# Performance work log

Measured on AMD Instinct MI355X. Metric: run time of the kernel, lower is better.

The kernel has to match this reference:

```python
import jax, jax.numpy as jnp
import numpy as np
import math

M, DIN, DTGT = 65536, 256, 256   # feature count and feature dims
S, SD_IN, SD_TGT = 64, 256, 256  # num_slots, in_slot_dim, tgt_slot_dim
ITERS = 3
H_IN = 128                        # mlp_in hidden (hardcoded 128 in source)
H_TGT = SD_TGT if SD_TGT > 128 else 128  # mlp_tgt hidden

ARGS = ["inputs", "target", "in_slots", "tgt_slots",
        "ln_in_g", "ln_in_b", "ln_tgt_g", "ln_tgt_b",
        "Wk", "bk", "Wv", "bv", "Wvt", "bvt",
        "ln_slots_g", "ln_slots_b", "Wq", "bq",
        "gru_in_Wih", "gru_in_Whh", "gru_in_bih", "gru_in_bhh",
        "gru_tgt_Wih", "gru_tgt_Whh", "gru_tgt_bih", "gru_tgt_bhh",
        "ln_mi_g", "ln_mi_b", "mi_W1", "mi_b1", "mi_W2", "mi_b2",
        "ln_mt_g", "ln_mt_b", "mt_W1", "mt_b1", "mt_W2", "mt_b2"]


def _ln(x, g, b):
    m = jnp.mean(x, axis=-1, keepdims=True)
    v = jnp.var(x, axis=-1, keepdims=True)
    return (x - m) * jax.lax.rsqrt(v + 1e-5) * g + b


def _gru(x, h, Wih, Whh, bih, bhh):
    # torch.nn.GRUCell semantics; Wih: (D, 3H), Whh: (H, 3H)
    H = h.shape[-1]
    gi = x @ Wih + bih
    gh = h @ Whh + bhh
    r = jax.nn.sigmoid(gi[:, :H] + gh[:, :H])
    z = jax.nn.sigmoid(gi[:, H:2 * H] + gh[:, H:2 * H])
    n = jnp.tanh(gi[:, 2 * H:] + r * gh[:, 2 * H:])
    return (1.0 - z) * n + z * h


def _forward(inputs, target, in_slots, tgt_slots,
             ln_in_g, ln_in_b, ln_tgt_g, ln_tgt_b,
             Wk, bk, Wv, bv, Wvt, bvt,
             ln_slots_g, ln_slots_b, Wq, bq,
             gru_in_Wih, gru_in_Whh, gru_in_bih, gru_in_bhh,
             gru_tgt_Wih, gru_tgt_Whh, gru_tgt_bih, gru_tgt_bhh,
             ln_mi_g, ln_mi_b, mi_W1, mi_b1, mi_W2, mi_b2,
             ln_mt_g, ln_mt_b, mt_W1, mt_b1, mt_W2, mt_b2):
    inputs_norm = _ln(inputs, ln_in_g, ln_in_b)          # [M, DIN]
    in_k = inputs_norm @ Wk + bk                          # [M, SD_IN]
    in_v = inputs_norm @ Wv + bv                          # [M, SD_IN]
    tgt_v = _ln(target, ln_tgt_g, ln_tgt_b) @ Wvt + bvt   # [M, SD_TGT]
    scale = 1.0 / math.sqrt(in_k.shape[1])
    attn = None
    for _ in range(ITERS):
        q = _ln(in_slots, ln_slots_g, ln_slots_b) @ Wq + bq   # [S, SD_IN]
        logits = (q @ in_k.T) * scale                          # [S, M]
        attn = jax.nn.softmax(logits, axis=0)                  # softmax over SLOTS (dim=0)
        in_up = attn @ in_v                                    # [S, SD_IN]
        tgt_up = attn @ tgt_v                                  # [S, SD_TGT]
        in_slots = _gru(in_up, in_slots, gru_in_Wih, gru_in_Whh, gru_in_bih, gru_in_bhh)
        tgt_slots = _gru(tgt_up, tgt_slots, gru_tgt_Wih, gru_tgt_Whh, gru_tgt_bih, gru_tgt_bhh)
        in_slots = in_slots + (jax.nn.relu(_ln(in_slots, ln_mi_g, ln_mi_b) @ mi_W1 + mi_b1) @ mi_W2 + mi_b2)
        tgt_slots = tgt_slots + (jax.nn.relu(_ln(tgt_slots, ln_mt_g, ln_mt_b) @ mt_W1 + mt_b1) @ mt_W2 + mt_b2)
    return (in_slots, tgt_slots, attn)


def setup_inputs() -> dict:
    key = jax.random.key(0)
    ks = iter(jax.random.split(key, 64))
    rn = lambda shape, s=1.0: jax.random.normal(next(ks), shape, dtype=jnp.float32) * s
    w = 0.02
    d = {
        "inputs": rn((M, DIN)),
        "target": rn((M, DTGT)),
        "in_slots": rn((S, SD_IN)),
        "tgt_slots": rn((S, SD_TGT)),
        "ln_in_g": jnp.ones((DIN,)), "ln_in_b": jnp.zeros((DIN,)),
        "ln_tgt_g": jnp.ones((DTGT,)), "ln_tgt_b": jnp.zeros((DTGT,)),
        "Wk": rn((DIN, SD_IN), w), "bk": jnp.zeros((SD_IN,)),
        "Wv": rn((DIN, SD_IN), w), "bv": jnp.zeros((SD_IN,)),
        "Wvt": rn((DTGT, SD_TGT), w), "bvt": jnp.zeros((SD_TGT,)),
        "ln_slots_g": jnp.ones((SD_IN,)), "ln_slots_b": jnp.zeros((SD_IN,)),
        "Wq": rn((SD_IN, SD_IN), w), "bq": jnp.zeros((SD_IN,)),
        "gru_in_Wih": rn((SD_IN, 3 * SD_IN), w), "gru_in_Whh": rn((SD_IN, 3 * SD_IN), w),
        "gru_in_bih": jnp.zeros((3 * SD_IN,)), "gru_in_bhh": jnp.zeros((3 * SD_IN,)),
        "gru_tgt_Wih": rn((SD_TGT, 3 * SD_TGT), w), "gru_tgt_Whh": rn((SD_TGT, 3 * SD_TGT), w),
        "gru_tgt_bih": jnp.zeros((3 * SD_TGT,)), "gru_tgt_bhh": jnp.zeros((3 * SD_TGT,)),
        "ln_mi_g": jnp.ones((SD_IN,)), "ln_mi_b": jnp.zeros((SD_IN,)),
        "mi_W1": rn((SD_IN, H_IN), w), "mi_b1": jnp.zeros((H_IN,)),
        "mi_W2": rn((H_IN, SD_IN), w), "mi_b2": jnp.zeros((SD_IN,)),
        "ln_mt_g": jnp.ones((SD_TGT,)), "ln_mt_b": jnp.zeros((SD_TGT,)),
        "mt_W1": rn((SD_TGT, H_TGT), w), "mt_b1": jnp.zeros((H_TGT,)),
        "mt_W2": rn((H_TGT, SD_TGT), w), "mt_b2": jnp.zeros((SD_TGT,)),
    }
    return {k: d[k] for k in ARGS}


def reference(inputs, target, in_slots, tgt_slots,
              ln_in_g, ln_in_b, ln_tgt_g, ln_tgt_b,
              Wk, bk, Wv, bv, Wvt, bvt,
              ln_slots_g, ln_slots_b, Wq, bq,
              gru_in_Wih, gru_in_Whh, gru_in_bih, gru_in_bhh,
              gru_tgt_Wih, gru_tgt_Whh, gru_tgt_bih, gru_tgt_bhh,
              ln_mi_g, ln_mi_b, mi_W1, mi_b1, mi_W2, mi_b2,
              ln_mt_g, ln_mt_b, mt_W1, mt_b1, mt_W2, mt_b2):
    return _forward(inputs, target, in_slots, tgt_slots,
                    ln_in_g, ln_in_b, ln_tgt_g, ln_tgt_b,
                    Wk, bk, Wv, bv, Wvt, bvt,
                    ln_slots_g, ln_slots_b, Wq, bq,
                    gru_in_Wih, gru_in_Whh, gru_in_bih, gru_in_bhh,
                    gru_tgt_Wih, gru_tgt_Whh, gru_tgt_bih, gru_tgt_bhh,
                    ln_mi_g, ln_mi_b, mi_W1, mi_b1, mi_W2, mi_b2,
                    ln_mt_g, ln_mt_b, mt_W1, mt_b1, mt_W2, mt_b2)
```

## Files before the change

kernel.cpp:

```cpp
#include <hip/hip_runtime.h>
#include <hip/hip_bf16.h>
#include <math.h>

typedef __bf16 bf16_t;
typedef __bf16 bf16x8 __attribute__((ext_vector_type(8)));
typedef __bf16 bf16x4 __attribute__((ext_vector_type(4)));
typedef float f32x4 __attribute__((ext_vector_type(4)));

#define DEVI __device__ __forceinline__

DEVI f32x4 mfma16(bf16x8 a, bf16x8 b, f32x4 c) {
  return __builtin_amdgcn_mfma_f32_16x16x32_bf16(a, b, c, 0, 0, 0);
}
DEVI bf16x8 ld8(const bf16_t* p) { return *reinterpret_cast<const bf16x8*>(p); }


struct WtArgs { const float* s0; const float* s1; const float* s2; const float* s3;
                const float* s4; const float* s5; const float* s6; const float* s7;
                const float* s8; const float* s9; const float* s10; const float* s11; };

__global__ __launch_bounds__(256) void k_wtrans(WtArgs A, bf16_t* __restrict__ wt,
                                                const float* __restrict__ g_in,
                                                const float* __restrict__ g_tgt) {
  constexpr int offs[12] = {0,65536,131072,196608,262144,458752,655360,851968,
                            1048576,1081344,1114112,1179648};
  constexpr int Ks[12]   = {256,256,256,256,256,256,256,256,256,128,256,256};
  constexpr int Ns[12]   = {256,256,256,256,768,768,768,768,128,256,256,256};
  const int m = blockIdx.y;
  const int K = Ks[m], N = Ns[m];
  const int tn = N >> 6;
  const int tile = blockIdx.x;
  if (tile >= (K >> 6) * tn) return;
  const int tk = tile / tn, tc = tile - tk * tn;
  const float* sp;
  switch (m) {
    case 0: sp = A.s0; break; case 1: sp = A.s1; break; case 2: sp = A.s2; break;
    case 3: sp = A.s3; break; case 4: sp = A.s4; break; case 5: sp = A.s5; break;
    case 6: sp = A.s6; break; case 7: sp = A.s7; break; case 8: sp = A.s8; break;
    case 9: sp = A.s9; break; case 10: sp = A.s10; break; default: sp = A.s11; break;
  }
  const float* gv = (m == 2) ? g_tgt : ((m < 2) ? g_in : nullptr);
  __shared__ float ts[64][65];
  const int t = threadIdx.x;
  const int k0 = tk * 64, n0 = tc * 64;
  {
    const int c = t & 63, rq = t >> 6;
    #pragma unroll
    for (int i = 0; i < 16; ++i) {
      const int r = rq * 16 + i;
      float val = sp[(size_t)(k0 + r) * N + n0 + c];
      if (gv) val *= gv[k0 + r];
      ts[r][c] = val;
    }
  }
  __syncthreads();
  bf16_t* dst = wt + offs[m];
  const int n_l = t & 63, kq = t >> 6;
  #pragma unroll
  for (int h = 0; h < 2; ++h) {
    const int k_l = kq * 16 + h * 8;
    bf16x8 pk;
    #pragma unroll
    for (int e = 0; e < 8; ++e) pk[e] = (bf16_t)ts[k_l + e][n_l];
    const int n_g = n0 + n_l, k_g = k0 + k_l;
    const int nt = n_g >> 4, kc = k_g >> 5;
    const int lane = (((k_g >> 3) & 3) << 4) + (n_g & 15);
    *reinterpret_cast<bf16x8*>(dst + (((size_t)(nt * (K >> 5) + kc)) << 9) + lane * 8) = pk;
  }
}

__global__ __launch_bounds__(256) void k_bias(
    const float* __restrict__ Wk, const float* __restrict__ Wv, const float* __restrict__ Wvt,
    const float* __restrict__ b_in, const float* __restrict__ b_tgt,
    const float* __restrict__ bk, const float* __restrict__ bv, const float* __restrict__ bvt,
    float* __restrict__ out) {
  const int which = blockIdx.x;
  const float* W = which == 0 ? Wk : (which == 1 ? Wv : Wvt);
  const float* bvec = which == 2 ? b_tgt : b_in;
  const float* bias = which == 0 ? bk : (which == 1 ? bv : bvt);
  const int n = threadIdx.x;
  float sum = bias[n];
  for (int k = 0; k < 256; ++k) sum += bvec[k] * W[(size_t)k * 256 + n];
  out[which * 256 + n] = sum;
}

__global__ __launch_bounds__(256) void k_init(const float* __restrict__ in_slots,
                                              const float* __restrict__ tgt_slots,
                                              float* __restrict__ h_f32,
                                              bf16_t* __restrict__ h_bf) {
  int idx = blockIdx.x * 256 + threadIdx.x;
  int side = idx >> 14, j = idx & 16383;
  int s = j >> 8, d = j & 255;
  float x = (side ? tgt_slots : in_slots)[j];
  h_f32[idx] = x;
  h_bf[side*16384 + (((s>>4)*8 + (d>>5))<<9) + ((d>>3)&3)*128 + (s&15)*8 + (d&7)] = (bf16_t)x;
}

DEVI void gemm_pass(const bf16_t* aFl, const bf16_t* __restrict__ WF,
                    int w, int l, f32x4 acc[4][4]) {
  #pragma unroll 1
  for (int ks = 0; ks < 8; ++ks) {
    bf16x8 a[4], b[4];
    #pragma unroll
    for (int mt = 0; mt < 4; ++mt) a[mt] = ld8(aFl + ((mt*8 + ks) << 9) + l*8);
    #pragma unroll
    for (int dt = 0; dt < 4; ++dt) b[dt] = ld8(WF + (((size_t)((w*4 + dt)*8 + ks)) << 9) + l*8);
    #pragma unroll
    for (int mt = 0; mt < 4; ++mt)
      #pragma unroll
      for (int dt = 0; dt < 4; ++dt) acc[mt][dt] = mfma16(a[mt], b[dt], acc[mt][dt]);
  }
}

__global__ __launch_bounds__(256) void k_phaseA(
    const float* __restrict__ inputs, const float* __restrict__ target,
    const bf16_t* __restrict__ wkF, const bf16_t* __restrict__ wvF, const bf16_t* __restrict__ wvtF,
    const float* __restrict__ bfold,
    bf16_t* __restrict__ in_kF, bf16_t* __restrict__ in_vF, bf16_t* __restrict__ tgt_vF) {
  const int side = blockIdx.y;
  const int m0 = blockIdx.x * 64;
  const int t = threadIdx.x, l = t & 63, w = t >> 6;
  const int l16 = l & 15, l4 = l >> 4;
  __shared__ __align__(16) bf16_t aF[16384];

  {
    const float* src = side ? target : inputs;
    const int row = m0 + w*16 + l16;
    const float* srcp = src + (size_t)row * 256 + l4 * 8;
    float4 xa[8], xb[8];
    #pragma unroll
    for (int j = 0; j < 8; ++j) {
      xa[j] = *reinterpret_cast<const float4*>(srcp + j*32);
      xb[j] = *reinterpret_cast<const float4*>(srcp + j*32 + 4);
    }
    float s1 = 0.f, s2 = 0.f;
    #pragma unroll
    for (int j = 0; j < 8; ++j) {
      s1 += xa[j].x + xa[j].y + xa[j].z + xa[j].w + xb[j].x + xb[j].y + xb[j].z + xb[j].w;
      s2 += xa[j].x*xa[j].x + xa[j].y*xa[j].y + xa[j].z*xa[j].z + xa[j].w*xa[j].w
          + xb[j].x*xb[j].x + xb[j].y*xb[j].y + xb[j].z*xb[j].z + xb[j].w*xb[j].w;
    }
    s1 += __shfl_xor(s1, 16); s1 += __shfl_xor(s1, 32);
    s2 += __shfl_xor(s2, 16); s2 += __shfl_xor(s2, 32);
    const float mean = s1 * (1.f/256.f);
    const float rstd = rsqrtf(s2 * (1.f/256.f) - mean*mean + 1e-5f);
    #pragma unroll
    for (int j = 0; j < 8; ++j) {
      bf16x8 pk;
      pk[0] = (bf16_t)((xa[j].x - mean) * rstd);
      pk[1] = (bf16_t)((xa[j].y - mean) * rstd);
      pk[2] = (bf16_t)((xa[j].z - mean) * rstd);
      pk[3] = (bf16_t)((xa[j].w - mean) * rstd);
      pk[4] = (bf16_t)((xb[j].x - mean) * rstd);
      pk[5] = (bf16_t)((xb[j].y - mean) * rstd);
      pk[6] = (bf16_t)((xb[j].z - mean) * rstd);
      pk[7] = (bf16_t)((xb[j].w - mean) * rstd);
      *reinterpret_cast<bf16x8*>(aF + ((w*8 + j) << 9) + l*8) = pk;
    }
  }
  __syncthreads();

  if (side == 0) {
    {
      f32x4 acc[4][4] = {};
      gemm_pass(aF, wkF, w, l, acc);
      #pragma unroll
      for (int mt = 0; mt < 4; ++mt) {
        const int mtg = blockIdx.x*4 + mt;
        #pragma unroll
        for (int dt = 0; dt < 4; ++dt) {
          const int dtg = w*4 + dt;
          const float bias = bfold[dtg*16 + l16];
          bf16_t* bp = in_kF + (((size_t)(mtg*8 + (dtg>>1))) << 9)
                       + ((dtg&1)*2 + (l16>>3))*128 + (l16&7);
          #pragma unroll
          for (int rr = 0; rr < 4; ++rr)
            bp[(l4*4 + rr)*8] = (bf16_t)(acc[mt][dt][rr] + bias);
        }
      }
    }
    {
      f32x4 acc[4][4] = {};
      gemm_pass(aF, wvF, w, l, acc);
      #pragma unroll
      for (int mt = 0; mt < 4; ++mt) {
        const int mcg = blockIdx.x*2 + (mt>>1);
        #pragma unroll
        for (int dt = 0; dt < 4; ++dt) {
          const int dtg = w*4 + dt;
          const float bias = bfold[256 + dtg*16 + l16];
          bf16x4 pk;
          #pragma unroll
          for (int rr = 0; rr < 4; ++rr) pk[rr] = (bf16_t)(acc[mt][dt][rr] + bias);
          *reinterpret_cast<bf16x4*>(in_vF + (((size_t)(dtg*2048 + mcg)) << 9)
              + ((mt&1)*2 + (l4>>1))*128 + l16*8 + (l4&1)*4) = pk;
        }
      }
    }
  } else {
    f32x4 acc[4][4] = {};
    gemm_pass(aF, wvtF, w, l, acc);
    #pragma unroll
    for (int mt = 0; mt < 4; ++mt) {
      const int mcg = blockIdx.x*2 + (mt>>1);
      #pragma unroll
      for (int dt = 0; dt < 4; ++dt) {
        const int dtg = w*4 + dt;
        const float bias = bfold[512 + dtg*16 + l16];
        bf16x4 pk;
        #pragma unroll
        for (int rr = 0; rr < 4; ++rr) pk[rr] = (bf16_t)(acc[mt][dt][rr] + bias);
        *reinterpret_cast<bf16x4*>(tgt_vF + (((size_t)(dtg*2048 + mcg)) << 9)
            + ((mt&1)*2 + (l4>>1))*128 + l16*8 + (l4&1)*4) = pk;
      }
    }
  }
}

__global__ __launch_bounds__(256) void k_q(
    const float* __restrict__ h_in,
    const float* __restrict__ ln_g, const float* __restrict__ ln_b,
    const bf16_t* __restrict__ wqF, const float* __restrict__ bq,
    bf16_t* __restrict__ q_bf) {
  __shared__ __align__(16) bf16_t anorm[64][264];
  const int t = threadIdx.x, l = t & 63, w = t >> 6;
  const float4 g4 = *reinterpret_cast<const float4*>(ln_g + l * 4);
  const float4 b4 = *reinterpret_cast<const float4*>(ln_b + l * 4);
  float4 v[16];
  #pragma unroll
  for (int i = 0; i < 16; ++i)
    v[i] = *reinterpret_cast<const float4*>(h_in + (size_t)(w*16 + i) * 256 + l * 4);
  #pragma unroll
  for (int i = 0; i < 16; ++i) {
    float s1 = v[i].x + v[i].y + v[i].z + v[i].w;
    float s2 = v[i].x*v[i].x + v[i].y*v[i].y + v[i].z*v[i].z + v[i].w*v[i].w;
    #pragma unroll
    for (int msk = 1; msk < 64; msk <<= 1) { s1 += __shfl_xor(s1, msk); s2 += __shfl_xor(s2, msk); }
    const float mean = s1 * (1.f/256.f);
    const float rstd = rsqrtf(s2 * (1.f/256.f) - mean*mean + 1e-5f);
    bf16x4 pk;
    pk[0] = (bf16_t)((v[i].x - mean) * rstd * g4.x + b4.x);
    pk[1] = (bf16_t)((v[i].y - mean) * rstd * g4.y + b4.y);
    pk[2] = (bf16_t)((v[i].z - mean) * rstd * g4.z + b4.z);
    pk[3] = (bf16_t)((v[i].w - mean) * rstd * g4.w + b4.w);
    *reinterpret_cast<bf16x4*>(&anorm[w*16 + i][l*4]) = pk;
  }
  __syncthreads();
  const int l16 = l & 15, l4 = l >> 4;
  f32x4 acc[4][4] = {};
  for (int ks = 0; ks < 8; ++ks) {
    const int k = ks*32 + l4*8;
    bf16x8 a[4], b[4];
    #pragma unroll
    for (int mi = 0; mi < 4; ++mi) a[mi] = ld8(&anorm[mi*16 + l16][k]);
    #pragma unroll
    for (int ni = 0; ni < 4; ++ni) b[ni] = ld8(wqF + (((size_t)((w*4 + ni)*8 + ks)) << 9) + l*8);
    #pragma unroll
    for (int mi = 0; mi < 4; ++mi)
      #pragma unroll
      for (int ni = 0; ni < 4; ++ni) acc[mi][ni] = mfma16(a[mi], b[ni], acc[mi][ni]);
  }
  #pragma unroll
  for (int mi = 0; mi < 4; ++mi)
    #pragma unroll
    for (int ni = 0; ni < 4; ++ni) {
      const int d = w*64 + ni*16 + l16;
      const float bias = bq[d];
      bf16_t* outp = q_bf + (((size_t)(mi*8 + w*2 + (ni>>1))) << 9) + ((ni&1)*2 + (l16>>3))*128 + (l16&7);
      #pragma unroll
      for (int rr = 0; rr < 4; ++rr)
        outp[(l4*4 + rr)*8] = (bf16_t)((acc[mi][ni][rr] + bias) * 0.0625f);
    }
}

__global__ __launch_bounds__(256) void k_logits(
    const bf16_t* __restrict__ q_bf, const bf16_t* __restrict__ in_kF,
    bf16_t* __restrict__ attnF, float* __restrict__ attn_f32, int write_f32) {
  __shared__ __align__(16) bf16_t stg[4][64][68];
  const int t = threadIdx.x, l = t & 63, w = t >> 6, l16 = l & 15, l4 = l >> 4;
  const int m0 = blockIdx.x * 256 + w * 64;
  f32x4 acc[4][4] = {};
  for (int ks = 0; ks < 8; ++ks) {
    bf16x8 a[4], b[4];
    #pragma unroll
    for (int mi = 0; mi < 4; ++mi) a[mi] = ld8(q_bf + (((size_t)(mi*8 + ks)) << 9) + l*8);
    #pragma unroll
    for (int ni = 0; ni < 4; ++ni)
      b[ni] = ld8(in_kF + (((size_t)((blockIdx.x*16 + w*4 + ni)*8 + ks)) << 9) + l*8);
    #pragma unroll
    for (int mi = 0; mi < 4; ++mi)
      #pragma unroll
      for (int ni = 0; ni < 4; ++ni) acc[mi][ni] = mfma16(a[mi], b[ni], acc[mi][ni]);
  }
  #pragma unroll
  for (int ni = 0; ni < 4; ++ni) {
    float mx = -3.0e38f;
    #pragma unroll
    for (int mi = 0; mi < 4; ++mi)
      #pragma unroll
      for (int rr = 0; rr < 4; ++rr) mx = fmaxf(mx, acc[mi][ni][rr]);
    mx = fmaxf(mx, __shfl_xor(mx, 16));
    mx = fmaxf(mx, __shfl_xor(mx, 32));
    float sm = 0.f;
    #pragma unroll
    for (int mi = 0; mi < 4; ++mi)
      #pragma unroll
      for (int rr = 0; rr < 4; ++rr) {
        float ev = __expf(acc[mi][ni][rr] - mx);
        acc[mi][ni][rr] = ev; sm += ev;
      }
    sm += __shfl_xor(sm, 16);
    sm += __shfl_xor(sm, 32);
    const float inv = 1.0f / sm;
    #pragma unroll
    for (int mi = 0; mi < 4; ++mi)
      #pragma unroll
      for (int rr = 0; rr < 4; ++rr) acc[mi][ni][rr] *= inv;
  }
  #pragma unroll
  for (int mi = 0; mi < 4; ++mi)
    #pragma unroll
    for (int ni = 0; ni < 4; ++ni)
      #pragma unroll
      for (int rr = 0; rr < 4; ++rr) {
        stg[w][mi*16 + l4*4 + rr][ni*16 + l16] = (bf16_t)acc[mi][ni][rr];
        if (write_f32) {
          const int s = mi*16 + l4*4 + rr;
          attn_f32[(size_t)s*65536 + (m0 + ni*16 + l16)] = acc[mi][ni][rr];
        }
      }
  #pragma unroll
  for (int mi = 0; mi < 4; ++mi)
    #pragma unroll
    for (int mc = 0; mc < 2; ++mc) {
      bf16x8 vv = *reinterpret_cast<const bf16x8*>(&stg[w][mi*16 + l16][mc*32 + l4*8]);
      *reinterpret_cast<bf16x8*>(attnF +
          ((((size_t)mi)*2048 + (blockIdx.x*8 + w*2 + mc)) << 9) + l*8) = vv;
    }
}

__global__ __launch_bounds__(256) void k_pv(
    const bf16_t* __restrict__ attnF,
    const bf16_t* __restrict__ in_vF, const bf16_t* __restrict__ tgt_vF,
    bf16_t* __restrict__ p_in, bf16_t* __restrict__ p_tgt) {
  const int c = blockIdx.x, side = blockIdx.y;
  const bf16_t* V = side ? tgt_vF : in_vF;
  bf16_t* P = side ? p_tgt : p_in;
  const int t = threadIdx.x, l = t & 63, w = t >> 6, l16 = l & 15, l4 = l >> 4;
  f32x4 acc[4][4] = {};
  for (int ks = 0; ks < 16; ++ks) {
    const size_t mc = c*16 + ks;
    bf16x8 a[4], b[4];
    #pragma unroll
    for (int mi = 0; mi < 4; ++mi) a[mi] = ld8(attnF + ((((size_t)mi)*2048 + mc) << 9) + l*8);
    #pragma unroll
    for (int ni = 0; ni < 4; ++ni) b[ni] = ld8(V + ((((size_t)(w*4 + ni))*2048 + mc) << 9) + l*8);
    #pragma unroll
    for (int mi = 0; mi < 4; ++mi)
      #pragma unroll
      for (int ni = 0; ni < 4; ++ni) acc[mi][ni] = mfma16(a[mi], b[ni], acc[mi][ni]);
  }
  #pragma unroll
  for (int mi = 0; mi < 4; ++mi)
    #pragma unroll
    for (int ni = 0; ni < 4; ++ni) {
      const int d = w*64 + ni*16 + l16;
      #pragma unroll
      for (int rr = 0; rr < 4; ++rr) {
        const int s = mi*16 + l4*4 + rr;
        P[(size_t)c*16384 + s*256 + d] = (bf16_t)acc[mi][ni][rr];
      }
    }
}

__global__ __launch_bounds__(256) void k_pvred(
    const bf16_t* __restrict__ p_in, const bf16_t* __restrict__ p_tgt,
    bf16_t* __restrict__ upF) {
  const int b = blockIdx.x;
  const int side = b >> 6, s = b & 63;
  const int d = threadIdx.x;
  const bf16_t* P = (side ? p_tgt : p_in) + s*256 + d;
  float sum = 0.f;
  #pragma unroll 8
  for (int cc = 0; cc < 128; ++cc) sum += (float)P[(size_t)cc * 16384];
  upF[side*16384 + (((s>>4)*8 + (d>>5))<<9) + ((d>>3)&3)*128 + (s&15)*8 + (d&7)] = (bf16_t)sum;
}

__global__ __launch_bounds__(256) void k_gates(
    const bf16_t* __restrict__ upF, const bf16_t* __restrict__ h_bf,
    const bf16_t* __restrict__ wihF_in, const bf16_t* __restrict__ whhF_in,
    const bf16_t* __restrict__ wihF_tgt, const bf16_t* __restrict__ whhF_tgt,
    const float* __restrict__ bih_in, const float* __restrict__ bhh_in,
    const float* __restrict__ bih_tgt, const float* __restrict__ bhh_tgt,
    float* __restrict__ gi, float* __restrict__ gh) {
  const int nchunk = blockIdx.x, which = blockIdx.y, side = blockIdx.z;
  const bf16_t* Aop = (which ? h_bf : upF) + side*16384;
  const bf16_t* WF = side ? (which ? whhF_tgt : wihF_tgt) : (which ? whhF_in : wihF_in);
  const float* bias = side ? (which ? bhh_tgt : bih_tgt) : (which ? bhh_in : bih_in);
  float* out = (which ? gh : gi) + side*49152;
  const int t = threadIdx.x, l = t & 63, w = t >> 6, l16 = l & 15, l4 = l >> 4;
  const int n0 = nchunk*256 + w*64;
  f32x4 acc[4][4] = {};
  for (int ks = 0; ks < 8; ++ks) {
    bf16x8 a[4], b[4];
    #pragma unroll
    for (int mi = 0; mi < 4; ++mi) a[mi] = ld8(Aop + (((size_t)(mi*8 + ks)) << 9) + l*8);
    #pragma unroll
    for (int ni = 0; ni < 4; ++ni)
      b[ni] = ld8(WF + (((size_t)((nchunk*16 + w*4 + ni)*8 + ks)) << 9) + l*8);
    #pragma unroll
    for (int mi = 0; mi < 4; ++mi)
      #pragma unroll
      for (int ni = 0; ni < 4; ++ni) acc[mi][ni] = mfma16(a[mi], b[ni], acc[mi][ni]);
  }
  #pragma unroll
  for (int mi = 0; mi < 4; ++mi)
    #pragma unroll
    for (int ni = 0; ni < 4; ++ni) {
      const int n = n0 + ni*16 + l16;
      const float bb = bias[n];
      #pragma unroll
      for (int rr = 0; rr < 4; ++rr) {
        const int s = mi*16 + l4*4 + rr;
        out[(size_t)s*768 + n] = acc[mi][ni][rr] + bb;
      }
    }
}

__global__ __launch_bounds__(256) void k_gru_ln(
    const float* __restrict__ gi, const float* __restrict__ gh,
    const float* __restrict__ h_f32,
    const float* __restrict__ ln_mi_g, const float* __restrict__ ln_mi_b,
    const float* __restrict__ ln_mt_g, const float* __restrict__ ln_mt_b,
    float* __restrict__ hp_f32, bf16_t* __restrict__ hpnF) {
  const int s = blockIdx.x, side = blockIdx.y;
  const int d = threadIdx.x;
  const float* GI = gi + side*49152 + s*768;
  const float* GH = gh + side*49152 + s*768;
  const float hv = h_f32[side*16384 + s*256 + d];
  const float rg = 1.f / (1.f + __expf(-(GI[d] + GH[d])));
  const float zg = 1.f / (1.f + __expf(-(GI[256 + d] + GH[256 + d])));
  const float ng = tanhf(GI[512 + d] + rg * GH[512 + d]);
  const float hp = (1.f - zg) * ng + zg * hv;
  float a = hp, b2 = hp * hp;
  #pragma unroll
  for (int msk = 1; msk < 64; msk <<= 1) { a += __shfl_xor(a, msk); b2 += __shfl_xor(b2, msk); }
  __shared__ float reda[4], redb[4];
  const int w = d >> 6, lid = d & 63;
  if (lid == 0) { reda[w] = a; redb[w] = b2; }
  __syncthreads();
  const float S1 = reda[0] + reda[1] + reda[2] + reda[3];
  const float S2 = redb[0] + redb[1] + redb[2] + redb[3];
  const float mean = S1 * (1.f/256.f);
  const float rstd = rsqrtf(S2 * (1.f/256.f) - mean*mean + 1e-5f);
  const float* g = side ? ln_mt_g : ln_mi_g;
  const float* bb = side ? ln_mt_b : ln_mi_b;
  const float nv = (hp - mean) * rstd * g[d] + bb[d];
  hp_f32[side*16384 + s*256 + d] = hp;
  hpnF[side*16384 + (((s>>4)*8 + (d>>5))<<9) + ((d>>3)&3)*128 + (s&15)*8 + (d&7)] = (bf16_t)nv;
}

__global__ __launch_bounds__(256) void k_mlpq(
    const bf16_t* __restrict__ hpnF,
    const bf16_t* __restrict__ w1F_in, const bf16_t* __restrict__ w1F_tgt,
    const float* __restrict__ b1_in, const float* __restrict__ b1_tgt,
    const bf16_t* __restrict__ w2F_in, const bf16_t* __restrict__ w2F_tgt,
    const float* __restrict__ b2_in, const float* __restrict__ b2_tgt,
    const float* __restrict__ hp_f32,
    float* __restrict__ h_f32, bf16_t* __restrict__ h_bf, float* __restrict__ slots_out,
    const float* __restrict__ ln_sg, const float* __restrict__ ln_sb,
    const bf16_t* __restrict__ wqF, const float* __restrict__ bq,
    bf16_t* __restrict__ q_bf, int make_q) {
  const int side = blockIdx.x;
  __shared__ __align__(16) bf16_t hid[64][264];
  const int t = threadIdx.x, l = t & 63, w = t >> 6, l16 = l & 15, l4 = l >> 4;
  const int NH = side ? 256 : 128;
  {
    const bf16_t* Aop = hpnF + side*16384;
    const bf16_t* WF = side ? w1F_tgt : w1F_in;
    const float* b1 = side ? b1_tgt : b1_in;
    const int ntiles = NH >> 6;
    for (int nt = 0; nt < ntiles; ++nt) {
      const int n0 = w*(NH>>2) + nt*16;
      f32x4 acc[4] = {};
      for (int ks = 0; ks < 8; ++ks) {
        bf16x8 b = ld8(WF + (((size_t)((n0>>4)*8 + ks)) << 9) + l*8);
        #pragma unroll
        for (int mt = 0; mt < 4; ++mt)
          acc[mt] = mfma16(ld8(Aop + (((size_t)(mt*8 + ks)) << 9) + l*8), b, acc[mt]);
      }
      const float bb = b1[n0 + l16];
      #pragma unroll
      for (int mt = 0; mt < 4; ++mt)
        #pragma unroll
        for (int rr = 0; rr < 4; ++rr) {
          const int s = mt*16 + l4*4 + rr;
          hid[s][n0 + l16] = (bf16_t)fmaxf(acc[mt][rr] + bb, 0.f);
        }
    }
  }
  __syncthreads();
  {
    const bf16_t* WF = side ? w2F_tgt : w2F_in;
    const float* b2 = side ? b2_tgt : b2_in;
    const int ksteps = NH >> 5;
    #pragma unroll
    for (int nt = 0; nt < 4; ++nt) {
      const int n0 = w*64 + nt*16;
      f32x4 acc[4] = {};
      for (int ks = 0; ks < ksteps; ++ks) {
        const int k = ks*32 + l4*8;
        bf16x8 b = ld8(WF + (((size_t)((n0>>4)*ksteps + ks)) << 9) + l*8);
        #pragma unroll
        for (int mt = 0; mt < 4; ++mt)
          acc[mt] = mfma16(ld8(&hid[mt*16 + l16][k]), b, acc[mt]);
      }
      const int n = n0 + l16;
      const float bb = b2[n];
      #pragma unroll
      for (int mt = 0; mt < 4; ++mt)
        #pragma unroll
        for (int rr = 0; rr < 4; ++rr) {
          const int s = mt*16 + l4*4 + rr;
          const int idx = side*16384 + s*256 + n;
          const float val = acc[mt][rr] + bb + hp_f32[idx];
          h_f32[idx] = val;
          slots_out[idx] = val;
          h_bf[side*16384 + (((s>>4)*8 + (n>>5))<<9) + ((n>>3)&3)*128 + (s&15)*8 + (n&7)] = (bf16_t)val;
        }
    }
  }
  if (!make_q || side != 0) return;
  __syncthreads();
  {
    for (int i = 0; i < 16; ++i) {
      const int s = w*16 + i;
      float4 x = *reinterpret_cast<const float4*>(h_f32 + s*256 + 4*l);
      float a = x.x + x.y + x.z + x.w;
      float b2s = x.x*x.x + x.y*x.y + x.z*x.z + x.w*x.w;
      #pragma unroll
      for (int msk = 1; msk < 64; msk <<= 1) { a += __shfl_xor(a, msk); b2s += __shfl_xor(b2s, msk); }
      const float mean = a * (1.f/256.f);
      const float rstd = rsqrtf(b2s * (1.f/256.f) - mean*mean + 1e-5f);
      float4 g4 = *reinterpret_cast<const float4*>(ln_sg + 4*l);
      float4 bb4 = *reinterpret_cast<const float4*>(ln_sb + 4*l);
      bf16x4 pk;
      pk[0] = (bf16_t)((x.x - mean) * rstd * g4.x + bb4.x);
      pk[1] = (bf16_t)((x.y - mean) * rstd * g4.y + bb4.y);
      pk[2] = (bf16_t)((x.z - mean) * rstd * g4.z + bb4.z);
      pk[3] = (bf16_t)((x.w - mean) * rstd * g4.w + bb4.w);
      *reinterpret_cast<bf16x4*>(&hid[s][4*l]) = pk;
    }
  }
  __syncthreads();
  {
    #pragma unroll
    for (int nt = 0; nt < 4; ++nt) {
      const int n0 = w*64 + nt*16;
      f32x4 acc[4] = {};
      for (int ks = 0; ks < 8; ++ks) {
        const int k = ks*32 + l4*8;
        bf16x8 b = ld8(wqF + (((size_t)((n0>>4)*8 + ks)) << 9) + l*8);
        #pragma unroll
        for (int mt = 0; mt < 4; ++mt)
          acc[mt] = mfma16(ld8(&hid[mt*16 + l16][k]), b, acc[mt]);
      }
      const int d = n0 + l16;
      const float bb = bq[d];
      #pragma unroll
      for (int mt = 0; mt < 4; ++mt) {
        bf16_t* op = q_bf + (((size_t)(mt*8 + (d>>5))) << 9) + ((d>>3)&3)*128 + (d&7);
        #pragma unroll
        for (int rr = 0; rr < 4; ++rr)
          op[(l4*4 + rr)*8] = (bf16_t)((acc[mt][rr] + bb) * 0.0625f);
      }
    }
  }
}

extern "C" void kernel_launch(void* const* d_in, const int* in_sizes, int n_in,
                              void* d_out, int out_size, void* d_ws, size_t ws_size,
                              hipStream_t stream) {
  (void)in_sizes; (void)n_in; (void)out_size; (void)ws_size;
  const float* inputs     = (const float*)d_in[0];
  const float* target     = (const float*)d_in[1];
  const float* in_slots   = (const float*)d_in[2];
  const float* tgt_slots  = (const float*)d_in[3];
  const float* ln_in_g    = (const float*)d_in[4];
  const float* ln_in_b    = (const float*)d_in[5];
  const float* ln_tgt_g   = (const float*)d_in[6];
  const float* ln_tgt_b   = (const float*)d_in[7];
  const float* Wk  = (const float*)d_in[8];
  const float* bk  = (const float*)d_in[9];
  const float* Wv  = (const float*)d_in[10];
  const float* bv  = (const float*)d_in[11];
  const float* Wvt = (const float*)d_in[12];
  const float* bvt = (const float*)d_in[13];
  const float* ln_slots_g = (const float*)d_in[14];
  const float* ln_slots_b = (const float*)d_in[15];
  const float* Wq  = (const float*)d_in[16];
  const float* bq  = (const float*)d_in[17];
  const float* gru_in_Wih  = (const float*)d_in[18];
  const float* gru_in_Whh  = (const float*)d_in[19];
  const float* gru_in_bih  = (const float*)d_in[20];
  const float* gru_in_bhh  = (const float*)d_in[21];
  const float* gru_tgt_Wih = (const float*)d_in[22];
  const float* gru_tgt_Whh = (const float*)d_in[23];
  const float* gru_tgt_bih = (const float*)d_in[24];
  const float* gru_tgt_bhh = (const float*)d_in[25];
  const float* ln_mi_g = (const float*)d_in[26];
  const float* ln_mi_b = (const float*)d_in[27];
  const float* mi_W1 = (const float*)d_in[28];
  const float* mi_b1 = (const float*)d_in[29];
  const float* mi_W2 = (const float*)d_in[30];
  const float* mi_b2 = (const float*)d_in[31];
  const float* ln_mt_g = (const float*)d_in[32];
  const float* ln_mt_b = (const float*)d_in[33];
  const float* mt_W1 = (const float*)d_in[34];
  const float* mt_b1 = (const float*)d_in[35];
  const float* mt_W2 = (const float*)d_in[36];
  const float* mt_b2 = (const float*)d_in[37];

  char* ws = (char*)d_ws;
  bf16_t* wt      = (bf16_t*)(ws);
  bf16_t* in_kF   = (bf16_t*)(ws + 2490368ull);
  bf16_t* in_vF   = (bf16_t*)(ws + 36044800ull);
  bf16_t* tgt_vF  = (bf16_t*)(ws + 69599232ull);
  bf16_t* attnF   = (bf16_t*)(ws + 103153664ull);
  bf16_t* q_bf    = (bf16_t*)(ws + 111542272ull);
  bf16_t* h_bf    = (bf16_t*)(ws + 111575040ull);
  bf16_t* upF     = (bf16_t*)(ws + 111640576ull);
  bf16_t* hpnF    = (bf16_t*)(ws + 111673344ull);
  float*  h_f32   = (float*)(ws + 111706112ull);
  float*  hp_f32  = (float*)(ws + 111837184ull);
  float*  gi      = (float*)(ws + 111968256ull);
  float*  gh      = (float*)(ws + 112361472ull);
  bf16_t* p_in    = (bf16_t*)(ws + 112754688ull);
  bf16_t* p_tgt   = (bf16_t*)(ws + 116948992ull);
  float*  bfold   = (float*)(ws + 121143296ull);

  bf16_t* wkF = wt;
  bf16_t* wvF = wt + 65536;
  bf16_t* wvtF = wt + 131072;
  bf16_t* wqF = wt + 196608;
  bf16_t* wihF_in  = wt + 262144;
  bf16_t* whhF_in  = wt + 458752;
  bf16_t* wihF_tgt = wt + 655360;
  bf16_t* whhF_tgt = wt + 851968;
  bf16_t* w1F_in  = wt + 1048576;
  bf16_t* w2F_in  = wt + 1081344;
  bf16_t* w1F_tgt = wt + 1114112;
  bf16_t* w2F_tgt = wt + 1179648;

  float* attn_out = (float*)d_out + 32768;

  WtArgs wa = {Wk, Wv, Wvt, Wq, gru_in_Wih, gru_in_Whh, gru_tgt_Wih, gru_tgt_Whh,
               mi_W1, mi_W2, mt_W1, mt_W2};
  k_wtrans<<<dim3(48, 12), 256, 0, stream>>>(wa, wt, ln_in_g, ln_tgt_g);
  k_bias<<<3, 256, 0, stream>>>(Wk, Wv, Wvt, ln_in_b, ln_tgt_b, bk, bv, bvt, bfold);
  k_init<<<128, 256, 0, stream>>>(in_slots, tgt_slots, h_f32, h_bf);
  k_phaseA<<<dim3(1024, 2), 256, 0, stream>>>(inputs, target,
      wkF, wvF, wvtF, bfold, in_kF, in_vF, tgt_vF);
  k_q<<<1, 256, 0, stream>>>(h_f32, ln_slots_g, ln_slots_b, wqF, bq, q_bf);

  for (int it = 0; it < 3; ++it) {
    k_logits<<<256, 256, 0, stream>>>(q_bf, in_kF, attnF, attn_out, it == 2 ? 1 : 0);
    k_pv<<<dim3(128, 2), 256, 0, stream>>>(attnF, in_vF, tgt_vF, p_in, p_tgt);
    k_pvred<<<128, 256, 0, stream>>>(p_in, p_tgt, upF);
    k_gates<<<dim3(3, 2, 2), 256, 0, stream>>>(upF, h_bf, wihF_in, whhF_in,
        wihF_tgt, whhF_tgt, gru_in_bih, gru_in_bhh, gru_tgt_bih, gru_tgt_bhh, gi, gh);
    k_gru_ln<<<dim3(64, 2), 256, 0, stream>>>(gi, gh, h_f32, ln_mi_g, ln_mi_b,
        ln_mt_g, ln_mt_b, hp_f32, hpnF);
    k_mlpq<<<2, 256, 0, stream>>>(hpnF, w1F_in, w1F_tgt, mi_b1, mt_b1,
        w2F_in, w2F_tgt, mi_b2, mt_b2, hp_f32, h_f32, h_bf, (float*)d_out,
        ln_slots_g, ln_slots_b, wqF, bq, q_bf, it < 2 ? 1 : 0);
  }
}
```

Before: 322.6 us.

## Fuse logits/softmax with PV matmul and enlarge phaseA row tile

```diff
diff --git a/kernel.cpp b/kernel.cpp
--- a/kernel.cpp
+++ b/kernel.cpp
@@ -96,19 +96,19 @@
   h_bf[side*16384 + (((s>>4)*8 + (d>>5))<<9) + ((d>>3)&3)*128 + (s&15)*8 + (d&7)] = (bf16_t)x;
 }
 
-DEVI void gemm_pass(const bf16_t* aFl, const bf16_t* __restrict__ WF,
-                    int w, int l, f32x4 acc[4][4]) {
+DEVI void gemm_pass8(const bf16_t* aFl, const bf16_t* __restrict__ WF,
+                     int w, int l, f32x4 acc[8][4]) {
   #pragma unroll 1
   for (int ks = 0; ks < 8; ++ks) {
-    bf16x8 a[4], b[4];
-    #pragma unroll
-    for (int mt = 0; mt < 4; ++mt) a[mt] = ld8(aFl + ((mt*8 + ks) << 9) + l*8);
+    bf16x8 b[4];
     #pragma unroll
     for (int dt = 0; dt < 4; ++dt) b[dt] = ld8(WF + (((size_t)((w*4 + dt)*8 + ks)) << 9) + l*8);
     #pragma unroll
-    for (int mt = 0; mt < 4; ++mt)
-      #pragma unroll
-      for (int dt = 0; dt < 4; ++dt) acc[mt][dt] = mfma16(a[mt], b[dt], acc[mt][dt]);
+    for (int mt = 0; mt < 8; ++mt) {
+      bf16x8 a = ld8(aFl + ((mt*8 + ks) << 9) + l*8);
+      #pragma unroll
+      for (int dt = 0; dt < 4; ++dt) acc[mt][dt] = mfma16(a, b[dt], acc[mt][dt]);
+    }
   }
 }
 
@@ -118,14 +118,15 @@
     const float* __restrict__ bfold,
     bf16_t* __restrict__ in_kF, bf16_t* __restrict__ in_vF, bf16_t* __restrict__ tgt_vF) {
   const int side = blockIdx.y;
-  const int m0 = blockIdx.x * 64;
+  const int m0 = blockIdx.x * 128;
   const int t = threadIdx.x, l = t & 63, w = t >> 6;
   const int l16 = l & 15, l4 = l >> 4;
-  __shared__ __align__(16) bf16_t aF[16384];
-
-  {
-    const float* src = side ? target : inputs;
-    const int row = m0 + w*16 + l16;
+  __shared__ __align__(16) bf16_t aF[32768];
+
+  const float* src = side ? target : inputs;
+  #pragma unroll 1
+  for (int p = 0; p < 2; ++p) {
+    const int row = m0 + p*64 + w*16 + l16;
     const float* srcp = src + (size_t)row * 256 + l4 * 8;
     float4 xa[8], xb[8];
     #pragma unroll
@@ -155,18 +156,18 @@
       pk[5] = (bf16_t)((xb[j].y - mean) * rstd);
       pk[6] = (bf16_t)((xb[j].z - mean) * rstd);
       pk[7] = (bf16_t)((xb[j].w - mean) * rstd);
-      *reinterpret_cast<bf16x8*>(aF + ((w*8 + j) << 9) + l*8) = pk;
+      *reinterpret_cast<bf16x8*>(aF + (((p*4 + w)*8 + j) << 9) + l*8) = pk;
     }
   }
   __syncthreads();
 
   if (side == 0) {
     {
-      f32x4 acc[4][4] = {};
-      gemm_pass(aF, wkF, w, l, acc);
-      #pragma unroll
-      for (int mt = 0; mt < 4; ++mt) {
-        const int mtg = blockIdx.x*4 + mt;
+      f32x4 acc[8][4] = {};
+      gemm_pass8(aF, wkF, w, l, acc);
+      #pragma unroll
+      for (int mt = 0; mt < 8; ++mt) {
+        const int mtg = blockIdx.x*8 + mt;
         #pragma unroll
         for (int dt = 0; dt < 4; ++dt) {
           const int dtg = w*4 + dt;
@@ -180,11 +181,11 @@
       }
     }
     {
-      f32x4 acc[4][4] = {};
-      gemm_pass(aF, wvF, w, l, acc);
-      #pragma unroll
-      for (int mt = 0; mt < 4; ++mt) {
-        const int mcg = blockIdx.x*2 + (mt>>1);
+      f32x4 acc[8][4] = {};
+      gemm_pass8(aF, wvF, w, l, acc);
+      #pragma unroll
+      for (int mt = 0; mt < 8; ++mt) {
+        const int mcg = blockIdx.x*4 + (mt>>1);
         #pragma unroll
         for (int dt = 0; dt < 4; ++dt) {
           const int dtg = w*4 + dt;
@@ -198,11 +199,11 @@
       }
     }
   } else {
-    f32x4 acc[4][4] = {};
-    gemm_pass(aF, wvtF, w, l, acc);
-    #pragma unroll
-    for (int mt = 0; mt < 4; ++mt) {
-      const int mcg = blockIdx.x*2 + (mt>>1);
+    f32x4 acc[8][4] = {};
+    gemm_pass8(aF, wvtF, w, l, acc);
+    #pragma unroll
+    for (int mt = 0; mt < 8; ++mt) {
+      const int mcg = blockIdx.x*4 + (mt>>1);
       #pragma unroll
       for (int dt = 0; dt < 4; ++dt) {
         const int dtg = w*4 + dt;
@@ -273,92 +274,93 @@
     }
 }
 
-__global__ __launch_bounds__(256) void k_logits(
+__global__ __launch_bounds__(256) void k_attn(
     const bf16_t* __restrict__ q_bf, const bf16_t* __restrict__ in_kF,
-    bf16_t* __restrict__ attnF, float* __restrict__ attn_f32, int write_f32) {
-  __shared__ __align__(16) bf16_t stg[4][64][68];
-  const int t = threadIdx.x, l = t & 63, w = t >> 6, l16 = l & 15, l4 = l >> 4;
-  const int m0 = blockIdx.x * 256 + w * 64;
-  f32x4 acc[4][4] = {};
-  for (int ks = 0; ks < 8; ++ks) {
-    bf16x8 a[4], b[4];
-    #pragma unroll
-    for (int mi = 0; mi < 4; ++mi) a[mi] = ld8(q_bf + (((size_t)(mi*8 + ks)) << 9) + l*8);
-    #pragma unroll
-    for (int ni = 0; ni < 4; ++ni)
-      b[ni] = ld8(in_kF + (((size_t)((blockIdx.x*16 + w*4 + ni)*8 + ks)) << 9) + l*8);
-    #pragma unroll
-    for (int mi = 0; mi < 4; ++mi)
-      #pragma unroll
-      for (int ni = 0; ni < 4; ++ni) acc[mi][ni] = mfma16(a[mi], b[ni], acc[mi][ni]);
-  }
-  #pragma unroll
-  for (int ni = 0; ni < 4; ++ni) {
-    float mx = -3.0e38f;
-    #pragma unroll
-    for (int mi = 0; mi < 4; ++mi)
-      #pragma unroll
-      for (int rr = 0; rr < 4; ++rr) mx = fmaxf(mx, acc[mi][ni][rr]);
-    mx = fmaxf(mx, __shfl_xor(mx, 16));
-    mx = fmaxf(mx, __shfl_xor(mx, 32));
-    float sm = 0.f;
-    #pragma unroll
-    for (int mi = 0; mi < 4; ++mi)
-      #pragma unroll
-      for (int rr = 0; rr < 4; ++rr) {
-        float ev = __expf(acc[mi][ni][rr] - mx);
-        acc[mi][ni][rr] = ev; sm += ev;
-      }
-    sm += __shfl_xor(sm, 16);
-    sm += __shfl_xor(sm, 32);
-    const float inv = 1.0f / sm;
-    #pragma unroll
-    for (int mi = 0; mi < 4; ++mi)
-      #pragma unroll
-      for (int rr = 0; rr < 4; ++rr) acc[mi][ni][rr] *= inv;
-  }
-  #pragma unroll
-  for (int mi = 0; mi < 4; ++mi)
-    #pragma unroll
-    for (int ni = 0; ni < 4; ++ni)
-      #pragma unroll
-      for (int rr = 0; rr < 4; ++rr) {
-        stg[w][mi*16 + l4*4 + rr][ni*16 + l16] = (bf16_t)acc[mi][ni][rr];
-        if (write_f32) {
-          const int s = mi*16 + l4*4 + rr;
-          attn_f32[(size_t)s*65536 + (m0 + ni*16 + l16)] = acc[mi][ni][rr];
-        }
-      }
-  #pragma unroll
-  for (int mi = 0; mi < 4; ++mi)
-    #pragma unroll
-    for (int mc = 0; mc < 2; ++mc) {
-      bf16x8 vv = *reinterpret_cast<const bf16x8*>(&stg[w][mi*16 + l16][mc*32 + l4*8]);
-      *reinterpret_cast<bf16x8*>(attnF +
-          ((((size_t)mi)*2048 + (blockIdx.x*8 + w*2 + mc)) << 9) + l*8) = vv;
-    }
-}
-
-__global__ __launch_bounds__(256) void k_pv(
-    const bf16_t* __restrict__ attnF,
     const bf16_t* __restrict__ in_vF, const bf16_t* __restrict__ tgt_vF,
-    bf16_t* __restrict__ p_in, bf16_t* __restrict__ p_tgt) {
+    bf16_t* __restrict__ p_in, bf16_t* __restrict__ p_tgt,
+    float* __restrict__ attn_f32, int write_f32) {
   const int c = blockIdx.x, side = blockIdx.y;
   const bf16_t* V = side ? tgt_vF : in_vF;
   bf16_t* P = side ? p_tgt : p_in;
+  __shared__ __align__(16) bf16_t stg[4][64][68];
+  __shared__ __align__(16) bf16_t pl[16384];
   const int t = threadIdx.x, l = t & 63, w = t >> 6, l16 = l & 15, l4 = l >> 4;
-  f32x4 acc[4][4] = {};
-  for (int ks = 0; ks < 16; ++ks) {
-    const size_t mc = c*16 + ks;
+
+  {
+    f32x4 acc[4][4] = {};
+    for (int ks = 0; ks < 8; ++ks) {
+      bf16x8 a[4], b[4];
+      #pragma unroll
+      for (int mi = 0; mi < 4; ++mi) a[mi] = ld8(q_bf + (((size_t)(mi*8 + ks)) << 9) + l*8);
+      #pragma unroll
+      for (int ni = 0; ni < 4; ++ni)
+        b[ni] = ld8(in_kF + (((size_t)((c*16 + w*4 + ni)*8 + ks)) << 9) + l*8);
+      #pragma unroll
+      for (int mi = 0; mi < 4; ++mi)
+        #pragma unroll
+        for (int ni = 0; ni < 4; ++ni) acc[mi][ni] = mfma16(a[mi], b[ni], acc[mi][ni]);
+    }
+    #pragma unroll
+    for (int ni = 0; ni < 4; ++ni) {
+      float mx = -3.0e38f;
+      #pragma unroll
+      for (int mi = 0; mi < 4; ++mi)
+        #pragma unroll
+        for (int rr = 0; rr < 4; ++rr) mx = fmaxf(mx, acc[mi][ni][rr]);
+      mx = fmaxf(mx, __shfl_xor(mx, 16));
+      mx = fmaxf(mx, __shfl_xor(mx, 32));
+      float sm = 0.f;
+      #pragma unroll
+      for (int mi = 0; mi < 4; ++mi)
+        #pragma unroll
+        for (int rr = 0; rr < 4; ++rr) {
+          float ev = __expf(acc[mi][ni][rr] - mx);
+          acc[mi][ni][rr] = ev; sm += ev;
+        }
+      sm += __shfl_xor(sm, 16);
+      sm += __shfl_xor(sm, 32);
+      const float inv = 1.0f / sm;
+      #pragma unroll
+      for (int mi = 0; mi < 4; ++mi)
+        #pragma unroll
+        for (int rr = 0; rr < 4; ++rr) acc[mi][ni][rr] *= inv;
+    }
+    const int m0 = c*256 + w*64;
+    #pragma unroll
+    for (int mi = 0; mi < 4; ++mi)
+      #pragma unroll
+      for (int ni = 0; ni < 4; ++ni)
+        #pragma unroll
+        for (int rr = 0; rr < 4; ++rr) {
+          stg[w][mi*16 + l4*4 + rr][ni*16 + l16] = (bf16_t)acc[mi][ni][rr];
+          if (write_f32 && side == 0) {
+            const int s = mi*16 + l4*4 + rr;
+            attn_f32[(size_t)s*65536 + (m0 + ni*16 + l16)] = acc[mi][ni][rr];
+          }
+        }
+    #pragma unroll
+    for (int mi = 0; mi < 4; ++mi)
+      #pragma unroll
+      for (int mc = 0; mc < 2; ++mc) {
+        bf16x8 vv = *reinterpret_cast<const bf16x8*>(&stg[w][mi*16 + l16][mc*32 + l4*8]);
+        *reinterpret_cast<bf16x8*>(pl + ((mi*8 + (w*2 + mc)) << 9) + l*8) = vv;
+      }
+  }
+  __syncthreads();
+
+  f32x4 acc2[4][4] = {};
+  #pragma unroll 1
+  for (int ks = 0; ks < 8; ++ks) {
+    const size_t mc = (size_t)c*8 + ks;
     bf16x8 a[4], b[4];
     #pragma unroll
-    for (int mi = 0; mi < 4; ++mi) a[mi] = ld8(attnF + ((((size_t)mi)*2048 + mc) << 9) + l*8);
+    for (int mi = 0; mi < 4; ++mi) a[mi] = ld8(pl + ((mi*8 + ks) << 9) + l*8);
     #pragma unroll
     for (int ni = 0; ni < 4; ++ni) b[ni] = ld8(V + ((((size_t)(w*4 + ni))*2048 + mc) << 9) + l*8);
     #pragma unroll
     for (int mi = 0; mi < 4; ++mi)
       #pragma unroll
-      for (int ni = 0; ni < 4; ++ni) acc[mi][ni] = mfma16(a[mi], b[ni], acc[mi][ni]);
+      for (int ni = 0; ni < 4; ++ni) acc2[mi][ni] = mfma16(a[mi], b[ni], acc2[mi][ni]);
   }
   #pragma unroll
   for (int mi = 0; mi < 4; ++mi)
@@ -368,7 +370,7 @@
       #pragma unroll
       for (int rr = 0; rr < 4; ++rr) {
         const int s = mi*16 + l4*4 + rr;
-        P[(size_t)c*16384 + s*256 + d] = (bf16_t)acc[mi][ni][rr];
+        P[(size_t)c*16384 + s*256 + d] = (bf16_t)acc2[mi][ni][rr];
       }
     }
 }
@@ -382,7 +384,7 @@
   const bf16_t* P = (side ? p_tgt : p_in) + s*256 + d;
   float sum = 0.f;
   #pragma unroll 8
-  for (int cc = 0; cc < 128; ++cc) sum += (float)P[(size_t)cc * 16384];
+  for (int cc = 0; cc < 256; ++cc) sum += (float)P[(size_t)cc * 16384];
   upF[side*16384 + (((s>>4)*8 + (d>>5))<<9) + ((d>>3)&3)*128 + (s&15)*8 + (d&7)] = (bf16_t)sum;
 }
 
@@ -626,17 +628,16 @@
   bf16_t* in_kF   = (bf16_t*)(ws + 2490368ull);
   bf16_t* in_vF   = (bf16_t*)(ws + 36044800ull);
   bf16_t* tgt_vF  = (bf16_t*)(ws + 69599232ull);
-  bf16_t* attnF   = (bf16_t*)(ws + 103153664ull);
-  bf16_t* q_bf    = (bf16_t*)(ws + 111542272ull);
-  bf16_t* h_bf    = (bf16_t*)(ws + 111575040ull);
-  bf16_t* upF     = (bf16_t*)(ws + 111640576ull);
-  bf16_t* hpnF    = (bf16_t*)(ws + 111673344ull);
-  float*  h_f32   = (float*)(ws + 111706112ull);
-  float*  hp_f32  = (float*)(ws + 111837184ull);
-  float*  gi      = (float*)(ws + 111968256ull);
-  float*  gh      = (float*)(ws + 112361472ull);
-  bf16_t* p_in    = (bf16_t*)(ws + 112754688ull);
-  bf16_t* p_tgt   = (bf16_t*)(ws + 116948992ull);
+  bf16_t* q_bf    = (bf16_t*)(ws + 103153664ull);
+  bf16_t* h_bf    = (bf16_t*)(ws + 103186432ull);
+  bf16_t* upF     = (bf16_t*)(ws + 103251968ull);
+  bf16_t* hpnF    = (bf16_t*)(ws + 103284736ull);
+  float*  h_f32   = (float*)(ws + 103317504ull);
+  float*  hp_f32  = (float*)(ws + 103448576ull);
+  float*  gi      = (float*)(ws + 103579648ull);
+  float*  gh      = (float*)(ws + 103972864ull);
+  bf16_t* p_in    = (bf16_t*)(ws + 104366080ull);
+  bf16_t* p_tgt   = (bf16_t*)(ws + 112754688ull);
   float*  bfold   = (float*)(ws + 121143296ull);
 
   bf16_t* wkF = wt;
@@ -659,13 +660,13 @@
   k_wtrans<<<dim3(48, 12), 256, 0, stream>>>(wa, wt, ln_in_g, ln_tgt_g);
   k_bias<<<3, 256, 0, stream>>>(Wk, Wv, Wvt, ln_in_b, ln_tgt_b, bk, bv, bvt, bfold);
   k_init<<<128, 256, 0, stream>>>(in_slots, tgt_slots, h_f32, h_bf);
-  k_phaseA<<<dim3(1024, 2), 256, 0, stream>>>(inputs, target,
+  k_phaseA<<<dim3(512, 2), 256, 0, stream>>>(inputs, target,
       wkF, wvF, wvtF, bfold, in_kF, in_vF, tgt_vF);
   k_q<<<1, 256, 0, stream>>>(h_f32, ln_slots_g, ln_slots_b, wqF, bq, q_bf);
 
   for (int it = 0; it < 3; ++it) {
-    k_logits<<<256, 256, 0, stream>>>(q_bf, in_kF, attnF, attn_out, it == 2 ? 1 : 0);
-    k_pv<<<dim3(128, 2), 256, 0, stream>>>(attnF, in_vF, tgt_vF, p_in, p_tgt);
+    k_attn<<<dim3(256, 2), 256, 0, stream>>>(q_bf, in_kF, in_vF, tgt_vF,
+        p_in, p_tgt, attn_out, it == 2 ? 1 : 0);
     k_pvred<<<128, 256, 0, stream>>>(p_in, p_tgt, upF);
     k_gates<<<dim3(3, 2, 2), 256, 0, stream>>>(upF, h_bf, wihF_in, whhF_in,
         wihF_tgt, whhF_tgt, gru_in_bih, gru_in_bhh, gru_tgt_bih, gru_tgt_bhh, gi, gh);
```

After: 368.7 us. +14.3%, slower.

## Keep normalized rows in registers per wave in phaseA projection GEMM

Applied to the files above, without the earlier changes.

```diff
diff --git a/kernel.cpp b/kernel.cpp
--- a/kernel.cpp
+++ b/kernel.cpp
@@ -96,42 +96,27 @@
   h_bf[side*16384 + (((s>>4)*8 + (d>>5))<<9) + ((d>>3)&3)*128 + (s&15)*8 + (d&7)] = (bf16_t)x;
 }
 
-DEVI void gemm_pass(const bf16_t* aFl, const bf16_t* __restrict__ WF,
-                    int w, int l, f32x4 acc[4][4]) {
-  #pragma unroll 1
-  for (int ks = 0; ks < 8; ++ks) {
-    bf16x8 a[4], b[4];
-    #pragma unroll
-    for (int mt = 0; mt < 4; ++mt) a[mt] = ld8(aFl + ((mt*8 + ks) << 9) + l*8);
-    #pragma unroll
-    for (int dt = 0; dt < 4; ++dt) b[dt] = ld8(WF + (((size_t)((w*4 + dt)*8 + ks)) << 9) + l*8);
-    #pragma unroll
-    for (int mt = 0; mt < 4; ++mt)
-      #pragma unroll
-      for (int dt = 0; dt < 4; ++dt) acc[mt][dt] = mfma16(a[mt], b[dt], acc[mt][dt]);
-  }
-}
-
 __global__ __launch_bounds__(256) void k_phaseA(
     const float* __restrict__ inputs, const float* __restrict__ target,
     const bf16_t* __restrict__ wkF, const bf16_t* __restrict__ wvF, const bf16_t* __restrict__ wvtF,
     const float* __restrict__ bfold,
     bf16_t* __restrict__ in_kF, bf16_t* __restrict__ in_vF, bf16_t* __restrict__ tgt_vF) {
   const int side = blockIdx.y;
-  const int m0 = blockIdx.x * 64;
   const int t = threadIdx.x, l = t & 63, w = t >> 6;
   const int l16 = l & 15, l4 = l >> 4;
-  __shared__ __align__(16) bf16_t aF[16384];
-
-  {
-    const float* src = side ? target : inputs;
-    const int row = m0 + w*16 + l16;
-    const float* srcp = src + (size_t)row * 256 + l4 * 8;
+  const int mbase = blockIdx.x * 128 + w * 32;
+  const float* src = side ? target : inputs;
+
+  bf16x8 A[2][8];
+  #pragma unroll 1
+  for (int mt = 0; mt < 2; ++mt) {
+    const int row = mbase + mt*16 + l16;
+    const float* rp = src + (size_t)row * 256 + l4 * 8;
     float4 xa[8], xb[8];
     #pragma unroll
     for (int j = 0; j < 8; ++j) {
-      xa[j] = *reinterpret_cast<const float4*>(srcp + j*32);
-      xb[j] = *reinterpret_cast<const float4*>(srcp + j*32 + 4);
+      xa[j] = *reinterpret_cast<const float4*>(rp + j*32);
+      xb[j] = *reinterpret_cast<const float4*>(rp + j*32 + 4);
     }
     float s1 = 0.f, s2 = 0.f;
     #pragma unroll
@@ -155,63 +140,75 @@
       pk[5] = (bf16_t)((xb[j].y - mean) * rstd);
       pk[6] = (bf16_t)((xb[j].z - mean) * rstd);
       pk[7] = (bf16_t)((xb[j].w - mean) * rstd);
-      *reinterpret_cast<bf16x8*>(aF + ((w*8 + j) << 9) + l*8) = pk;
-    }
-  }
-  __syncthreads();
+      A[mt][j] = pk;
+    }
+  }
+
+  const int mtg0 = mbase >> 4;
+  const int mcg  = mbase >> 5;
 
   if (side == 0) {
-    {
-      f32x4 acc[4][4] = {};
-      gemm_pass(aF, wkF, w, l, acc);
-      #pragma unroll
-      for (int mt = 0; mt < 4; ++mt) {
-        const int mtg = blockIdx.x*4 + mt;
-        #pragma unroll
-        for (int dt = 0; dt < 4; ++dt) {
-          const int dtg = w*4 + dt;
-          const float bias = bfold[dtg*16 + l16];
-          bf16_t* bp = in_kF + (((size_t)(mtg*8 + (dtg>>1))) << 9)
-                       + ((dtg&1)*2 + (l16>>3))*128 + (l16&7);
-          #pragma unroll
-          for (int rr = 0; rr < 4; ++rr)
-            bp[(l4*4 + rr)*8] = (bf16_t)(acc[mt][dt][rr] + bias);
+    #pragma unroll 1
+    for (int nt = 0; nt < 16; ++nt) {
+      f32x4 a0 = {}, a1 = {};
+      #pragma unroll
+      for (int ks = 0; ks < 8; ++ks) {
+        bf16x8 b = ld8(wkF + (((size_t)(nt*8 + ks)) << 9) + l*8);
+        a0 = mfma16(A[0][ks], b, a0);
+        a1 = mfma16(A[1][ks], b, a1);
+      }
+      const float bias = bfold[nt*16 + l16];
+      #pragma unroll
+      for (int mt = 0; mt < 2; ++mt) {
+        const f32x4 av = mt ? a1 : a0;
+        bf16_t* bp = in_kF + (((size_t)((mtg0 + mt)*8 + (nt>>1))) << 9)
+                     + ((nt&1)*2 + (l16>>3))*128 + (l16&7);
+        #pragma unroll
+        for (int rr = 0; rr < 4; ++rr)
+          bp[(l4*4 + rr)*8] = (bf16_t)(av[rr] + bias);
+      }
+    }
+    #pragma unroll 1
+    for (int nt = 0; nt < 16; ++nt) {
+      f32x4 a0 = {}, a1 = {};
+      #pragma unroll
+      for (int ks = 0; ks < 8; ++ks) {
+        bf16x8 b = ld8(wvF + (((size_t)(nt*8 + ks)) << 9) + l*8);
+        a0 = mfma16(A[0][ks], b, a0);
+        a1 = mfma16(A[1][ks], b, a1);
+      }
+      const float bias = bfold[256 + nt*16 + l16];
+      bf16_t* outb = in_vF + (((size_t)(nt*2048 + mcg)) << 9) + l16*8;
+      #pragma unroll
+      for (int mt = 0; mt < 2; ++mt) {
+        const f32x4 av = mt ? a1 : a0;
+        #pragma unroll
+        for (int rr = 0; rr < 4; ++rr) {
+          const int mlo = mt*16 + l4*4 + rr;
+          outb[((mlo>>3)&3)*128 + (mlo&7)] = (bf16_t)(av[rr] + bias);
         }
       }
     }
-    {
-      f32x4 acc[4][4] = {};
-      gemm_pass(aF, wvF, w, l, acc);
-      #pragma unroll
-      for (int mt = 0; mt < 4; ++mt) {
-        const int mcg = blockIdx.x*2 + (mt>>1);
-        #pragma unroll
-        for (int dt = 0; dt < 4; ++dt) {
-          const int dtg = w*4 + dt;
-          const float bias = bfold[256 + dtg*16 + l16];
-          bf16x4 pk;
-          #pragma unroll
-          for (int rr = 0; rr < 4; ++rr) pk[rr] = (bf16_t)(acc[mt][dt][rr] + bias);
-          *reinterpret_cast<bf16x4*>(in_vF + (((size_t)(dtg*2048 + mcg)) << 9)
-              + ((mt&1)*2 + (l4>>1))*128 + l16*8 + (l4&1)*4) = pk;
+  } else {
+    #pragma unroll 1
+    for (int nt = 0; nt < 16; ++nt) {
+      f32x4 a0 = {}, a1 = {};
+      #pragma unroll
+      for (int ks = 0; ks < 8; ++ks) {
+        bf16x8 b = ld8(wvtF + (((size_t)(nt*8 + ks)) << 9) + l*8);
+        a0 = mfma16(A[0][ks], b, a0);
+        a1 = mfma16(A[1][ks], b, a1);
+      }
+      const float bias = bfold[512 + nt*16 + l16];
+      bf16_t* outb = tgt_vF + (((size_t)(nt*2048 + mcg)) << 9) + l16*8;
+      #pragma unroll
+      for (int mt = 0; mt < 2; ++mt) {
+        const f32x4 av = mt ? a1 : a0;
+        #pragma unroll
+        for (int rr = 0; rr < 4; ++rr) {
+          const int mlo = mt*16 + l4*4 + rr;
+          outb[((mlo>>3)&3)*128 + (mlo&7)] = (bf16_t)(av[rr] + bias);
         }
-      }
-    }
-  } else {
-    f32x4 acc[4][4] = {};
-    gemm_pass(aF, wvtF, w, l, acc);
-    #pragma unroll
-    for (int mt = 0; mt < 4; ++mt) {
-      const int mcg = blockIdx.x*2 + (mt>>1);
-      #pragma unroll
-      for (int dt = 0; dt < 4; ++dt) {
-        const int dtg = w*4 + dt;
-        const float bias = bfold[512 + dtg*16 + l16];
-        bf16x4 pk;
-        #pragma unroll
-        for (int rr = 0; rr < 4; ++rr) pk[rr] = (bf16_t)(acc[mt][dt][rr] + bias);
-        *reinterpret_cast<bf16x4*>(tgt_vF + (((size_t)(dtg*2048 + mcg)) << 9)
-            + ((mt&1)*2 + (l4>>1))*128 + l16*8 + (l4&1)*4) = pk;
       }
     }
   }
@@ -659,7 +656,7 @@
   k_wtrans<<<dim3(48, 12), 256, 0, stream>>>(wa, wt, ln_in_g, ln_tgt_g);
   k_bias<<<3, 256, 0, stream>>>(Wk, Wv, Wvt, ln_in_b, ln_tgt_b, bk, bv, bvt, bfold);
   k_init<<<128, 256, 0, stream>>>(in_slots, tgt_slots, h_f32, h_bf);
-  k_phaseA<<<dim3(1024, 2), 256, 0, stream>>>(inputs, target,
+  k_phaseA<<<dim3(512, 2), 256, 0, stream>>>(inputs, target,
       wkF, wvF, wvtF, bfold, in_kF, in_vF, tgt_vF);
   k_q<<<1, 256, 0, stream>>>(h_f32, ln_slots_g, ln_slots_b, wqF, bq, q_bf);
 
```

Measured after the change: 354.6 us. 1.1x slower.
